# Performance work log

Hardware: AMD Instinct MI355X
Metric: run time of the kernel (lower is better)

## Reference

```python
import jax, jax.numpy as jnp
import numpy as np

B, T, I, H, O = 64, 2048, 128, 512, 64
NOISE_STD = 0.0005
ALPHA = 0.1


def setup_inputs() -> dict:
    key = jax.random.key(0)
    k0, k1, k2, k3, k4 = jax.random.split(key, 5)
    return {
        "input": jax.random.normal(k0, (B, T, I), dtype=jnp.float32),
        "noise": jax.random.normal(k1, (B, T, H), dtype=jnp.float32),
        "wi": jax.random.normal(k2, (I, H), dtype=jnp.float32) * (1.0 / np.sqrt(I)).astype(np.float32),
        "wrec": jax.random.normal(k3, (H, H), dtype=jnp.float32) * (1.0 / np.sqrt(H)).astype(np.float32),
        "wout": jax.random.normal(k4, (H, O), dtype=jnp.float32) * (1.0 / np.sqrt(H)).astype(np.float32),
        "h0": jnp.zeros((H,), dtype=jnp.float32),
    }


def reference(input, noise, wi, wrec, wout, h0):
    b, t = input.shape[0], input.shape[1]
    # initial state broadcast over batch
    h_init = jnp.broadcast_to(h0, (b, h0.shape[0]))
    out0 = jnp.tanh(h0) @ wout  # [O] -- output at t=0 uses tanh(h0)

    # time-major slices for steps 0..T-2 (torch loop runs range(seq_len-1))
    xs = (jnp.swapaxes(input[:, :-1, :], 0, 1),  # [T-1, B, I]
          jnp.swapaxes(noise[:, :-1, :], 0, 1))  # [T-1, B, H]

    def step(h, xn):
        x, n = xn
        r = jnp.tanh(h)
        h = h + NOISE_STD * n + ALPHA * (-h + r @ wrec.T + x @ wi)
        return h, jnp.tanh(h) @ wout  # [B, O]

    _, outs = jax.lax.scan(step, h_init, xs)  # [T-1, B, O]
    out0b = jnp.broadcast_to(out0, (1, b, out0.shape[0]))
    return jnp.swapaxes(jnp.concatenate([out0b, outs], axis=0), 0, 1)  # [B, T, O]
```

## Files before the change

### kernel.cpp

```cpp
#include <hip/hip_runtime.h>
#include <stdint.h>

#define Bv 64
#define Tv 2048
#define Iv 128
#define Hv 512
#define Ov 64

typedef _Float16 half_t;
typedef _Float16 half2_t __attribute__((ext_vector_type(2)));

__device__ __forceinline__ float fdot2(unsigned int a, unsigned int b, float c) {
#if __has_builtin(__builtin_amdgcn_fdot2)
    return __builtin_amdgcn_fdot2(__builtin_bit_cast(half2_t, a),
                                  __builtin_bit_cast(half2_t, b), c, false);
#else
    half2_t ha = __builtin_bit_cast(half2_t, a);
    half2_t hb = __builtin_bit_cast(half2_t, b);
    return c + (float)ha.x * (float)hb.x + (float)ha.y * (float)hb.y;
#endif
}

__device__ __forceinline__ unsigned int pack2(float a, float b) {
    half2_t v; v.x = (half_t)a; v.y = (half_t)b;
    return __builtin_bit_cast(unsigned int, v);
}


__global__ void pack_wrA_k(const float* __restrict__ wrec, unsigned int* __restrict__ wp) {
    int idx = blockIdx.x * 256 + threadIdx.x;
    if (idx >= 180 * 512) return;
    int j = idx & 511, m = idx >> 9;
    wp[idx] = pack2(wrec[j * Hv + 2 * m], wrec[j * Hv + 2 * m + 1]);
}

__global__ void pack_wB_k(const float* __restrict__ wrec, unsigned int* __restrict__ wp) {
    int idx = blockIdx.x * 256 + threadIdx.x;
    if (idx >= 19 * 512 * 4) return;
    int c = idx & 3, j = (idx >> 2) & 511, g = idx >> 11;
    int k = 360 + 8 * g + 2 * c;
    wp[idx] = pack2(wrec[j * Hv + k], wrec[j * Hv + k + 1]);
}

__global__ void pack_wip_k(const float* __restrict__ wi, unsigned int* __restrict__ wp) {
    int idx = blockIdx.x * 256 + threadIdx.x;
    int j = idx & 511, m = idx >> 9;
    wp[idx] = pack2(wi[(2 * m) * Hv + j], wi[(2 * m + 1) * Hv + j]);
}

__global__ void pack_wop_k(const float* __restrict__ wout, uint4* __restrict__ wp) {
    int idx = blockIdx.x * 256 + threadIdx.x;
    if (idx >= 64 * 64) return;
    int o = idx & 63, g = idx >> 6;
    uint4 v;
    v.x = pack2(wout[(8 * g + 0) * Ov + o], wout[(8 * g + 1) * Ov + o]);
    v.y = pack2(wout[(8 * g + 2) * Ov + o], wout[(8 * g + 3) * Ov + o]);
    v.z = pack2(wout[(8 * g + 4) * Ov + o], wout[(8 * g + 5) * Ov + o]);
    v.w = pack2(wout[(8 * g + 6) * Ov + o], wout[(8 * g + 7) * Ov + o]);
    wp[idx] = v;
}

__global__ __launch_bounds__(512) void z_kernel(
    const float* __restrict__ x, const float* __restrict__ noise,
    const unsigned int* __restrict__ wip, half_t* __restrict__ zg)
{
    __shared__ uint4 xs[32 * 16];
    const int tid = threadIdx.x;
    const size_t bt0 = (size_t)blockIdx.x * 32;

    unsigned int wiR[64];
#pragma unroll
    for (int m = 0; m < 64; ++m) wiR[m] = wip[m * 512 + tid];

    for (int idx = tid; idx < 32 * 64; idx += 512) {
        int row = idx >> 6, m = idx & 63;
        float2 xv = ((const float2*)x)[(bt0 + row) * 64 + m];
        ((unsigned int*)xs)[idx] = pack2(xv.x, xv.y);
    }
    __syncthreads();

    for (int row = 0; row < 32; ++row) {
        float a0 = 0.f, a1 = 0.f, a2 = 0.f, a3 = 0.f;
#pragma unroll
        for (int g = 0; g < 16; ++g) {
            uint4 xv = xs[row * 16 + g];
            a0 = fdot2(wiR[4 * g + 0], xv.x, a0);
            a1 = fdot2(wiR[4 * g + 1], xv.y, a1);
            a2 = fdot2(wiR[4 * g + 2], xv.z, a2);
            a3 = fdot2(wiR[4 * g + 3], xv.w, a3);
        }
        float nv = noise[(bt0 + row) * 512 + tid];
        zg[(bt0 + row) * 512 + tid] = (half_t)(0.1f * ((a0 + a1) + (a2 + a3)) + 0.0005f * nv);
    }
}

__global__ __launch_bounds__(512) __attribute__((amdgpu_waves_per_eu(2, 2)))
void rnn_fast(
    const unsigned int* __restrict__ wrAg,
    const uint4* __restrict__ wBg,
    const half_t* __restrict__ zg,
    const float* __restrict__ h0,
    half_t* __restrict__ rstore)
{
    extern __shared__ unsigned char smem[];
    uint4* wlds = (uint4*)smem;
    half_t* s_r16 = (half_t*)(smem + 19 * 512 * 16);
    const uint4* s_r4 = (const uint4*)s_r16;

    const int tid = threadIdx.x;
    const int b = blockIdx.x;

    for (int i = tid; i < 19 * 512; i += 512) wlds[i] = wBg[i];

    unsigned int wrA[180];
#pragma unroll
    for (int m = 0; m < 180; ++m) wrA[m] = wrAg[m * 512 + tid];

    const half_t* zb = zg + (size_t)b * Tv * Hv;
    half_t* rb = rstore + (size_t)b * Tv * Hv;

    float h = h0[tid];
    half_t r0 = (half_t)tanhf(h);
    s_r16[tid] = r0;
    rb[tid] = r0;
    half_t zpf = zb[tid];
    __syncthreads();

    int cur = 0;
    for (int t = 0; t < Tv - 1; ++t) {
        half_t zc = zpf;
        zpf = zb[(size_t)(t + 1) * Hv + tid];

        const uint4* rq = s_r4 + cur * 64;
        float a0 = 0.f, a1 = 0.f, a2 = 0.f, a3 = 0.f;
#pragma unroll
        for (int q = 0; q < 45; ++q) {
            uint4 rv = rq[q];
            a0 = fdot2(wrA[4 * q + 0], rv.x, a0);
            a1 = fdot2(wrA[4 * q + 1], rv.y, a1);
            a2 = fdot2(wrA[4 * q + 2], rv.z, a2);
            a3 = fdot2(wrA[4 * q + 3], rv.w, a3);
        }
#pragma unroll
        for (int g = 0; g < 19; ++g) {
            uint4 rv = rq[45 + g];
            uint4 wv = wlds[g * 512 + tid];
            a0 = fdot2(wv.x, rv.x, a0);
            a1 = fdot2(wv.y, rv.y, a1);
            a2 = fdot2(wv.z, rv.z, a2);
            a3 = fdot2(wv.w, rv.w, a3);
        }
        float acc = (a0 + a1) + (a2 + a3);
        h = 0.9f * h + 0.1f * acc + (float)zc;
        half_t r = (half_t)tanhf(h);
        s_r16[(cur ^ 1) * 512 + tid] = r;
        rb[(size_t)(t + 1) * Hv + tid] = r;
        __syncthreads();
        cur ^= 1;
    }
}

__global__ __launch_bounds__(256) void out_kernel(
    const half_t* __restrict__ rstore, const uint4* __restrict__ wop4, float* __restrict__ out)
{
    __shared__ uint4 rr[32 * 64];
    const int tid = threadIdx.x;
    const int o = tid & 63, q = tid >> 6;
    const size_t bt0 = (size_t)blockIdx.x * 32;

    for (int idx = tid; idx < 32 * 64; idx += 256)
        rr[idx] = ((const uint4*)rstore)[bt0 * 64 + idx];
    __syncthreads();

    float acc[8] = {0.f, 0.f, 0.f, 0.f, 0.f, 0.f, 0.f, 0.f};
#pragma unroll 8
    for (int g = 0; g < 64; ++g) {
        uint4 wv = wop4[g * 64 + o];
#pragma unroll
        for (int i = 0; i < 8; ++i) {
            uint4 rv = rr[(q + 4 * i) * 64 + g];
            float a = fdot2(wv.x, rv.x, acc[i]);
            a = fdot2(wv.y, rv.y, a);
            a = fdot2(wv.z, rv.z, a);
            acc[i] = fdot2(wv.w, rv.w, a);
        }
    }
#pragma unroll
    for (int i = 0; i < 8; ++i)
        out[(bt0 + q + 4 * i) * Ov + o] = acc[i];
}

__global__ void pack_wrec_k(const float* __restrict__ wrec, unsigned int* __restrict__ wp) {
    int tid = blockIdx.x * 256 + threadIdx.x;
    int k = tid & 3, j = (tid >> 2) & 511, q = tid >> 11;
    int i0 = 8 * q + 2 * k;
    wp[tid] = pack2(wrec[j * Hv + i0], wrec[j * Hv + i0 + 1]);
}
__global__ void pack_wi_k(const float* __restrict__ wi, unsigned int* __restrict__ wp) {
    int tid = blockIdx.x * 256 + threadIdx.x;
    int k = tid & 3, j = (tid >> 2) & 511, q = tid >> 11;
    int i0 = 8 * q + 2 * k;
    wp[tid] = pack2(wi[i0 * Hv + j], wi[(i0 + 1) * Hv + j]);
}
__global__ void pack_wout_k(const float* __restrict__ wout, unsigned int* __restrict__ wp) {
    int tid = blockIdx.x * 256 + threadIdx.x;
    int o = tid & 63, m = tid >> 6;
    wp[tid] = pack2(wout[(2 * m) * Ov + o], wout[(2 * m + 1) * Ov + o]);
}
__global__ __launch_bounds__(512) void rnn_persistent(
    const float* __restrict__ x, const float* __restrict__ noise,
    const float* __restrict__ h0,
    const unsigned int* __restrict__ wrecp,
    const unsigned int* __restrict__ wip,
    const unsigned int* __restrict__ wop,
    float* __restrict__ out)
{
    __shared__ __align__(16) unsigned int s_r[2][256];
    __shared__ __align__(16) unsigned int s_x[64];
    const int tid = threadIdx.x;
    const int b = blockIdx.x;
    const int o = tid >> 3;
    const int g = tid & 7;
    const float* xb = x + (size_t)b * Tv * Iv;
    const float* nb = noise + (size_t)b * Tv * Hv;
    float* ob = out + (size_t)b * Tv * Ov;
    unsigned int wiReg[64];
#pragma unroll
    for (int m = 0; m < 64; ++m)
        wiReg[m] = wip[(((m >> 2) * Hv) + tid) * 4 + (m & 3)];
    unsigned int wo[32];
#pragma unroll
    for (int k = 0; k < 32; ++k)
        wo[k] = wop[(g * 32 + k) * Ov + o];
    float h = h0[tid];
    ((half_t*)&s_r[0][0])[tid] = (half_t)tanhf(h);
    __syncthreads();
    {
        float po = 0.f;
        const uint4* r2 = (const uint4*)&s_r[0][0];
#pragma unroll
        for (int k = 0; k < 8; ++k) {
            uint4 rv = r2[g * 8 + k];
            po = fdot2(wo[4 * k + 0], rv.x, po);
            po = fdot2(wo[4 * k + 1], rv.y, po);
            po = fdot2(wo[4 * k + 2], rv.z, po);
            po = fdot2(wo[4 * k + 3], rv.w, po);
        }
        po += __shfl_xor(po, 1, 64);
        po += __shfl_xor(po, 2, 64);
        po += __shfl_xor(po, 4, 64);
        if (g == 0) ob[o] = po;
    }
    const uint4* wr4 = (const uint4*)wrecp;
    int cur = 0;
    for (int t = 0; t < Tv - 1; ++t) {
        const int nxt = cur ^ 1;
        float nval = nb[t * Hv + tid];
        if (tid < Iv) ((half_t*)&s_x[0])[tid] = (half_t)xb[t * Iv + tid];
        __syncthreads();
        float acc = 0.f;
        const uint4* rr4 = (const uint4*)&s_r[cur][0];
#pragma unroll 8
        for (int q = 0; q < 64; ++q) {
            uint4 w = wr4[q * Hv + tid];
            uint4 r = rr4[q];
            acc = fdot2(w.x, r.x, acc);
            acc = fdot2(w.y, r.y, acc);
            acc = fdot2(w.z, r.z, acc);
            acc = fdot2(w.w, r.w, acc);
        }
        const uint4* xx4 = (const uint4*)&s_x[0];
#pragma unroll
        for (int m = 0; m < 16; ++m) {
            uint4 xv = xx4[m];
            acc = fdot2(wiReg[4 * m + 0], xv.x, acc);
            acc = fdot2(wiReg[4 * m + 1], xv.y, acc);
            acc = fdot2(wiReg[4 * m + 2], xv.z, acc);
            acc = fdot2(wiReg[4 * m + 3], xv.w, acc);
        }
        h = h + 0.0005f * nval + 0.1f * (acc - h);
        ((half_t*)&s_r[nxt][0])[tid] = (half_t)tanhf(h);
        __syncthreads();
        float po = 0.f;
        const uint4* r2 = (const uint4*)&s_r[nxt][0];
#pragma unroll
        for (int k = 0; k < 8; ++k) {
            uint4 rv = r2[g * 8 + k];
            po = fdot2(wo[4 * k + 0], rv.x, po);
            po = fdot2(wo[4 * k + 1], rv.y, po);
            po = fdot2(wo[4 * k + 2], rv.z, po);
            po = fdot2(wo[4 * k + 3], rv.w, po);
        }
        po += __shfl_xor(po, 1, 64);
        po += __shfl_xor(po, 2, 64);
        po += __shfl_xor(po, 4, 64);
        if (g == 0) ob[(t + 1) * Ov + o] = po;
        cur = nxt;
    }
}

extern "C" void kernel_launch(void* const* d_in, const int* in_sizes, int n_in,
                              void* d_out, int out_size, void* d_ws, size_t ws_size,
                              hipStream_t stream) {
    const float* input = (const float*)d_in[0];
    const float* noise = (const float*)d_in[1];
    const float* wi    = (const float*)d_in[2];
    const float* wrec  = (const float*)d_in[3];
    const float* wout  = (const float*)d_in[4];
    const float* h0    = (const float*)d_in[5];
    float* out = (float*)d_out;

    const size_t Z_OFF  = 0;
    const size_t R_OFF  = Z_OFF + 134217728;
    const size_t WA_OFF = R_OFF + 134217728;
    const size_t WB_OFF = WA_OFF + 368640;
    const size_t WI_OFF = WB_OFF + 155648;
    const size_t WO_OFF = WI_OFF + 131072;
    const size_t NEED   = WO_OFF + 65536;

    if (ws_size >= NEED) {
        unsigned char* ws = (unsigned char*)d_ws;
        half_t*       zg    = (half_t*)(ws + Z_OFF);
        half_t*       rsg   = (half_t*)(ws + R_OFF);
        unsigned int* wrAg  = (unsigned int*)(ws + WA_OFF);
        unsigned int* wBg   = (unsigned int*)(ws + WB_OFF);
        unsigned int* wipg  = (unsigned int*)(ws + WI_OFF);
        uint4*        wop4g = (uint4*)(ws + WO_OFF);

        hipLaunchKernelGGL(pack_wrA_k, dim3(360), dim3(256), 0, stream, wrec, wrAg);
        hipLaunchKernelGGL(pack_wB_k,  dim3(152), dim3(256), 0, stream, wrec, wBg);
        hipLaunchKernelGGL(pack_wip_k, dim3(128), dim3(256), 0, stream, wi, wipg);
        hipLaunchKernelGGL(pack_wop_k, dim3(16),  dim3(256), 0, stream, wout, wop4g);

        hipLaunchKernelGGL(z_kernel, dim3((Bv * Tv) / 32), dim3(512), 0, stream,
                           input, noise, wipg, zg);

        const int smem = 19 * 512 * 16 + 2 * 512 * 2;
        hipFuncSetAttribute((const void*)rnn_fast,
                            hipFuncAttributeMaxDynamicSharedMemorySize, smem);
        hipLaunchKernelGGL(rnn_fast, dim3(Bv), dim3(512), smem, stream,
                           wrAg, (const uint4*)wBg, zg, h0, rsg);

        hipLaunchKernelGGL(out_kernel, dim3((Bv * Tv) / 32), dim3(256), 0, stream,
                           rsg, wop4g, out);
    } else {
        unsigned int* wrecp = (unsigned int*)d_ws;
        unsigned int* wip   = wrecp + 64 * 512 * 4;
        unsigned int* wop   = wip   + 16 * 512 * 4;
        hipLaunchKernelGGL(pack_wrec_k, dim3(512), dim3(256), 0, stream, wrec, wrecp);
        hipLaunchKernelGGL(pack_wi_k,   dim3(128), dim3(256), 0, stream, wi, wip);
        hipLaunchKernelGGL(pack_wout_k, dim3(64),  dim3(256), 0, stream, wout, wop);
        hipLaunchKernelGGL(rnn_persistent, dim3(Bv), dim3(512), 0, stream,
                           input, noise, h0, wrecp, wip, wop, out);
    }
}
```

Baseline: 3.578 ms.

## Split recurrent dot product across lane quarters with skewed LDS state layout

Each wavefront's 64 lanes now form 4 k-slices × 16 output columns. Every thread computes partial sums for 4 outputs over a 128-wide slice of the hidden state, then reduces them with cross-lane shuffles. The shared hidden-state buffer uses a padded, skewed layout so each slice reads its own contiguous region, and the recurrent weights are repacked to match. The aim is to cut the number of LDS broadcast reads of the hidden state per step, at the cost of shuffle reductions and select logic on the serial critical path.

```diff
diff --git a/kernel.cpp b/kernel.cpp
--- a/kernel.cpp
+++ b/kernel.cpp
@@ -27,19 +27,26 @@
 }
 
 
-__global__ void pack_wrA_k(const float* __restrict__ wrec, unsigned int* __restrict__ wp) {
+__global__ void pack_wrA4_k(const float* __restrict__ wrec, unsigned int* __restrict__ wp) {
     int idx = blockIdx.x * 256 + threadIdx.x;
     if (idx >= 180 * 512) return;
-    int j = idx & 511, m = idx >> 9;
-    wp[idx] = pack2(wrec[j * Hv + 2 * m], wrec[j * Hv + 2 * m + 1]);
-}
-
-__global__ void pack_wB_k(const float* __restrict__ wrec, unsigned int* __restrict__ wp) {
+    int tid = idx & 511, row = idx >> 9;
+    int p = row / 45, m = row % 45;
+    int w = tid >> 6, lm = tid & 63, s = lm >> 4, u = lm & 15;
+    int j = 64 * w + u + 16 * p;
+    int k0 = 128 * s + 2 * m;
+    wp[idx] = pack2(wrec[j * Hv + k0], wrec[j * Hv + k0 + 1]);
+}
+
+__global__ void pack_wB4_k(const float* __restrict__ wrec, unsigned int* __restrict__ wp) {
     int idx = blockIdx.x * 256 + threadIdx.x;
     if (idx >= 19 * 512 * 4) return;
-    int c = idx & 3, j = (idx >> 2) & 511, g = idx >> 11;
-    int k = 360 + 8 * g + 2 * c;
-    wp[idx] = pack2(wrec[j * Hv + k], wrec[j * Hv + k + 1]);
+    int c = idx & 3, tid = (idx >> 2) & 511, g = idx >> 11;
+    int w = tid >> 6, lm = tid & 63, s = lm >> 4, u = lm & 15;
+    int j = 64 * w + u + 16 * c;
+    int m = 45 + g;
+    int k0 = 128 * s + 2 * m;
+    wp[idx] = pack2(wrec[j * Hv + k0], wrec[j * Hv + k0 + 1]);
 }
 
 __global__ void pack_wip_k(const float* __restrict__ wi, unsigned int* __restrict__ wp) {
@@ -94,7 +101,24 @@
     }
 }
 
-__global__ __launch_bounds__(512) __attribute__((amdgpu_waves_per_eu(2, 2)))
+#define RSKEW(q, j) ((q) * 1088 + ((j) >> 7) * 272 + ((j) & 127) * 2)
+
+#define STEP_REG(RU, M)                                   \
+    acc0 = fdot2(wrA[(M)], (RU), acc0);                   \
+    acc1 = fdot2(wrA[45 + (M)], (RU), acc1);              \
+    acc2 = fdot2(wrA[90 + (M)], (RU), acc2);              \
+    acc3 = fdot2(wrA[135 + (M)], (RU), acc3);
+
+#define STEP_LDS(RU, M)                                   \
+    {                                                     \
+        uint4 wv = wlds[((M) - 45) * 512 + tid];          \
+        acc0 = fdot2(wv.x, (RU), acc0);                   \
+        acc1 = fdot2(wv.y, (RU), acc1);                   \
+        acc2 = fdot2(wv.z, (RU), acc2);                   \
+        acc3 = fdot2(wv.w, (RU), acc3);                   \
+    }
+
+__global__ __attribute__((amdgpu_flat_work_group_size(512, 512), amdgpu_waves_per_eu(2, 2)))
 void rnn_fast(
     const unsigned int* __restrict__ wrAg,
     const uint4* __restrict__ wBg,
@@ -104,57 +128,75 @@
 {
     extern __shared__ unsigned char smem[];
     uint4* wlds = (uint4*)smem;
-    half_t* s_r16 = (half_t*)(smem + 19 * 512 * 16);
-    const uint4* s_r4 = (const uint4*)s_r16;
+    unsigned char* rbase = smem + 19 * 512 * 16;
 
     const int tid = threadIdx.x;
     const int b = blockIdx.x;
+    const int s = (tid >> 4) & 3;
+    const int jown = ((tid >> 6) << 6) + (tid & 15) + 16 * s;
 
     for (int i = tid; i < 19 * 512; i += 512) wlds[i] = wBg[i];
 
     unsigned int wrA[180];
 #pragma unroll
     for (int m = 0; m < 180; ++m) wrA[m] = wrAg[m * 512 + tid];
+    asm volatile("" ::: "memory");
 
     const half_t* zb = zg + (size_t)b * Tv * Hv;
     half_t* rb = rstore + (size_t)b * Tv * Hv;
 
-    float h = h0[tid];
+    float h = h0[jown];
     half_t r0 = (half_t)tanhf(h);
-    s_r16[tid] = r0;
-    rb[tid] = r0;
-    half_t zpf = zb[tid];
+    *(half_t*)(rbase + RSKEW(0, jown)) = r0;
+    rb[jown] = r0;
+    half_t zpf = zb[jown];
     __syncthreads();
 
     int cur = 0;
     for (int t = 0; t < Tv - 1; ++t) {
         half_t zc = zpf;
-        zpf = zb[(size_t)(t + 1) * Hv + tid];
-
-        const uint4* rq = s_r4 + cur * 64;
-        float a0 = 0.f, a1 = 0.f, a2 = 0.f, a3 = 0.f;
-#pragma unroll
-        for (int q = 0; q < 45; ++q) {
-            uint4 rv = rq[q];
-            a0 = fdot2(wrA[4 * q + 0], rv.x, a0);
-            a1 = fdot2(wrA[4 * q + 1], rv.y, a1);
-            a2 = fdot2(wrA[4 * q + 2], rv.z, a2);
-            a3 = fdot2(wrA[4 * q + 3], rv.w, a3);
-        }
-#pragma unroll
-        for (int g = 0; g < 19; ++g) {
-            uint4 rv = rq[45 + g];
-            uint4 wv = wlds[g * 512 + tid];
-            a0 = fdot2(wv.x, rv.x, a0);
-            a1 = fdot2(wv.y, rv.y, a1);
-            a2 = fdot2(wv.z, rv.z, a2);
-            a3 = fdot2(wv.w, rv.w, a3);
-        }
-        float acc = (a0 + a1) + (a2 + a3);
-        h = 0.9f * h + 0.1f * acc + (float)zc;
+        zpf = zb[(size_t)(t + 1) * Hv + jown];
+
+        const uint4* rq = (const uint4*)(rbase + cur * 1088 + s * 272);
+
+        float acc0 = 0.f, acc1 = 0.f, acc2 = 0.f, acc3 = 0.f;
+#pragma unroll
+        for (int g = 0; g < 11; ++g) {
+            uint4 rv = rq[g];
+            STEP_REG(rv.x, 4 * g + 0)
+            STEP_REG(rv.y, 4 * g + 1)
+            STEP_REG(rv.z, 4 * g + 2)
+            STEP_REG(rv.w, 4 * g + 3)
+        }
+        {
+            uint4 rv = rq[11];
+            STEP_REG(rv.x, 44)
+            STEP_LDS(rv.y, 45)
+            STEP_LDS(rv.z, 46)
+            STEP_LDS(rv.w, 47)
+        }
+#pragma unroll
+        for (int g = 12; g < 16; ++g) {
+            uint4 rv = rq[g];
+            STEP_LDS(rv.x, 4 * g + 0)
+            STEP_LDS(rv.y, 4 * g + 1)
+            STEP_LDS(rv.z, 4 * g + 2)
+            STEP_LDS(rv.w, 4 * g + 3)
+        }
+
+        acc0 += __shfl_xor(acc0, 16, 64); acc0 += __shfl_xor(acc0, 32, 64);
+        acc1 += __shfl_xor(acc1, 16, 64); acc1 += __shfl_xor(acc1, 32, 64);
+        acc2 += __shfl_xor(acc2, 16, 64); acc2 += __shfl_xor(acc2, 32, 64);
+        acc3 += __shfl_xor(acc3, 16, 64); acc3 += __shfl_xor(acc3, 32, 64);
+
+        float t01 = (s & 1) ? acc1 : acc0;
+        float t23 = (s & 1) ? acc3 : acc2;
+        float tot = (s & 2) ? t23 : t01;
+
+        h = 0.9f * h + 0.1f * tot + (float)zc;
         half_t r = (half_t)tanhf(h);
-        s_r16[(cur ^ 1) * 512 + tid] = r;
-        rb[(size_t)(t + 1) * Hv + tid] = r;
+        *(half_t*)(rbase + RSKEW(cur ^ 1, jown)) = r;
+        rb[(size_t)(t + 1) * Hv + jown] = r;
         __syncthreads();
         cur ^= 1;
     }
@@ -327,15 +369,15 @@
         unsigned int* wipg  = (unsigned int*)(ws + WI_OFF);
         uint4*        wop4g = (uint4*)(ws + WO_OFF);
 
-        hipLaunchKernelGGL(pack_wrA_k, dim3(360), dim3(256), 0, stream, wrec, wrAg);
-        hipLaunchKernelGGL(pack_wB_k,  dim3(152), dim3(256), 0, stream, wrec, wBg);
-        hipLaunchKernelGGL(pack_wip_k, dim3(128), dim3(256), 0, stream, wi, wipg);
-        hipLaunchKernelGGL(pack_wop_k, dim3(16),  dim3(256), 0, stream, wout, wop4g);
+        hipLaunchKernelGGL(pack_wrA4_k, dim3(360), dim3(256), 0, stream, wrec, wrAg);
+        hipLaunchKernelGGL(pack_wB4_k,  dim3(152), dim3(256), 0, stream, wrec, wBg);
+        hipLaunchKernelGGL(pack_wip_k,  dim3(128), dim3(256), 0, stream, wi, wipg);
+        hipLaunchKernelGGL(pack_wop_k,  dim3(16),  dim3(256), 0, stream, wout, wop4g);
 
         hipLaunchKernelGGL(z_kernel, dim3((Bv * Tv) / 32), dim3(512), 0, stream,
                            input, noise, wipg, zg);
 
-        const int smem = 19 * 512 * 16 + 2 * 512 * 2;
+        const int smem = 19 * 512 * 16 + 2 * 1088;
         hipFuncSetAttribute((const void*)rnn_fast,
                             hipFuncAttributeMaxDynamicSharedMemorySize, smem);
         hipLaunchKernelGGL(rnn_fast, dim3(Bv), dim3(512), smem, stream,
```

New measurement: 3.485 ms. -2.6%, faster.
